# Kernel tuning notes

Hardware: AMD Instinct MI355X
Metric: run time of the kernel (lower is better)

The kernel has to match this reference:

```python
import jax, jax.numpy as jnp
import numpy as np
import math

EMBED = 1024
HEADS = 16
HEAD_DIM = EMBED // HEADS


def setup_inputs() -> dict:
    key = jax.random.key(0)
    ks = jax.random.split(key, 9)
    B, S = 2, 2048
    query = jax.random.normal(ks[0], (B, S, EMBED), dtype=jnp.float32)
    key_t = jax.random.normal(ks[1], (B, S, EMBED), dtype=jnp.float32)
    value = jax.random.normal(ks[2], (B, S, EMBED), dtype=jnp.float32)
    mask = jax.random.randint(ks[3], (B, 1, S, S), 0, 2, dtype=jnp.int32)
    # nn.Linear(head_dim, head_dim, bias=False) weights: [out, in]
    sc = 1.0 / math.sqrt(HEAD_DIM)
    Wq = jax.random.uniform(ks[4], (HEAD_DIM, HEAD_DIM), jnp.float32, -sc, sc)
    Wk = jax.random.uniform(ks[5], (HEAD_DIM, HEAD_DIM), jnp.float32, -sc, sc)
    Wv = jax.random.uniform(ks[6], (HEAD_DIM, HEAD_DIM), jnp.float32, -sc, sc)
    so = 1.0 / math.sqrt(EMBED)
    Wo = jax.random.uniform(ks[7], (EMBED, EMBED), jnp.float32, -so, so)
    bo = jax.random.uniform(ks[8], (EMBED,), jnp.float32, -so, so)
    return {"query": query, "key": key_t, "value": value, "mask": mask,
            "Wq": Wq, "Wk": Wk, "Wv": Wv, "Wo": Wo, "bo": bo}


def reference(query, key, value, mask, Wq, Wk, Wv, Wo, bo):
    B, Sq, E = query.shape
    Sk = key.shape[1]
    H, D = HEADS, HEAD_DIM
    # Faithful raw reshape into heads (as in the torch source, no transpose)
    q = query.reshape(B, H, Sq, D)
    k = key.reshape(B, H, Sk, D)
    v = value.reshape(B, H, Sk, D)
    # per-head_dim Linear (bias-free): x @ W.T
    Q = jnp.einsum('bhsd,ed->bhse', q, Wq)
    K = jnp.einsum('bhsd,ed->bhse', k, Wk)
    V = jnp.einsum('bhsd,ed->bhse', v, Wv)
    scores = jnp.einsum('bhqd,bhkd->bhqk', Q, K)  # [B,H,Sq,Sk]
    scores = jnp.where(mask == 0, jnp.float32(-1e20), scores)
    # NOTE: source divides by sqrt(embed_size), not sqrt(head_dim)
    attn = jax.nn.softmax(scores / jnp.float32(math.sqrt(E)), axis=-1)
    out = jnp.einsum('bhqk,bhkd->bhqd', attn, V).reshape(B, Sq, H * D)
    return out @ Wo.T + bo
```

## Files before the change

kernel.cpp:

```cpp
#include <hip/hip_runtime.h>

typedef __attribute__((ext_vector_type(8))) short short8;
typedef __attribute__((ext_vector_type(4))) float f32x4;
typedef __attribute__((ext_vector_type(2))) int int2v;
typedef __attribute__((ext_vector_type(4))) int int4v;

__device__ __forceinline__ short f2bf(float f) {
  unsigned u = __builtin_bit_cast(unsigned, f);
  u += 0x7fff + ((u >> 16) & 1);
  return (short)(u >> 16);
}

__device__ __forceinline__ int pk2bf(float lo, float hi) {
#if defined(__gfx950__) && __has_builtin(__builtin_amdgcn_cvt_pk_bf16_f32)
  typedef __attribute__((ext_vector_type(2))) __bf16 bf16x2;
  bf16x2 v = __builtin_amdgcn_cvt_pk_bf16_f32(lo, hi);
  return __builtin_bit_cast(int, v);
#else
  return (int)(unsigned short)(short)f2bf(lo) | (((int)f2bf(hi)) << 16);
#endif
}

__device__ __forceinline__ int pktr(float lo, float hi) {
#if __has_builtin(__builtin_amdgcn_perm)
  return (int)__builtin_amdgcn_perm(__builtin_bit_cast(unsigned, hi),
                                    __builtin_bit_cast(unsigned, lo), 0x07060302u);
#else
  return (int)(__builtin_bit_cast(unsigned, lo) >> 16) |
         (int)(__builtin_bit_cast(unsigned, hi) & 0xffff0000u);
#endif
}

__device__ __forceinline__ short8 pack8(f32x4 a, f32x4 b) {
  int4v t;
  t.x = pk2bf(a[0], a[1]);
  t.y = pk2bf(a[2], a[3]);
  t.z = pk2bf(b[0], b[1]);
  t.w = pk2bf(b[2], b[3]);
  return __builtin_bit_cast(short8, t);
}

__device__ __forceinline__ float fand(float p, int m) {
  return __builtin_bit_cast(float, __builtin_bit_cast(int, p) & m);
}

__device__ __forceinline__ int bmask(unsigned w, int bit) {
#if __has_builtin(__builtin_amdgcn_sbfe)
  return __builtin_amdgcn_sbfe((int)w, bit, 1);
#else
  return ((int)(w << (31 - bit))) >> 31;
#endif
}

__device__ __forceinline__ float fexp2(float x) {
#if __has_builtin(__builtin_amdgcn_exp2f)
  return __builtin_amdgcn_exp2f(x);
#else
  return exp2f(x);
#endif
}

__device__ __forceinline__ void glds16(const short* g, short* lbase, int lane) {
#if __has_builtin(__builtin_amdgcn_global_load_lds)
  __builtin_amdgcn_global_load_lds(
      (const __attribute__((address_space(1))) unsigned int*)g,
      (__attribute__((address_space(3))) unsigned int*)lbase, 16, 0, 0);
#else
  *(short8*)(lbase + lane * 8) = *(const short8*)g;
#endif
}

__global__ __launch_bounds__(256) void projqkv(const float* __restrict__ q,
                                               const float* __restrict__ k,
                                               const float* __restrict__ v,
                                               const float* __restrict__ Wq,
                                               const float* __restrict__ Wk,
                                               const float* __restrict__ Wv,
                                               short* __restrict__ Qp,
                                               short* __restrict__ Kp,
                                               short* __restrict__ Vtp) {
  const int bid = blockIdx.x;
  const int tid = threadIdx.x;

  __shared__ short xt[64][72];
  __shared__ short ot[64][72];
  const int mode = bid >> 10;
  const int bt = bid & 1023;
  const float* X;
  const float* W;
  float scale;
  if (mode == 0) { X = q; W = Wq; scale = 0.045084220f; }
  else if (mode == 1) { X = k; W = Wk; scale = 1.0f; }
  else { X = v; W = Wv; scale = 1.0f; }

  const int r0 = bt * 64;
  const int row = tid >> 2, seg = (tid & 3) * 16;
  const f32x4* xs = (const f32x4*)(X + (r0 + row) * 64 + seg);
  const f32x4 x0 = xs[0], x1 = xs[1], x2 = xs[2], x3 = xs[3];
  *(short8*)&xt[row][seg] = pack8(x0, x1);
  *(short8*)&xt[row][seg + 8] = pack8(x2, x3);
  __syncthreads();

  const int lane = tid & 63, wave = tid >> 6;
  const int m16 = lane & 15, quad = lane >> 4;

  const short8 a0 = *(const short8*)&xt[wave * 16 + m16][quad * 8];
  const short8 a1 = *(const short8*)&xt[wave * 16 + m16][32 + quad * 8];

  f32x4 acc[4];
#pragma unroll
  for (int nt = 0; nt < 4; ++nt) {
    const f32x4* wp0 = (const f32x4*)&W[(nt * 16 + m16) * 64 + quad * 8];
    const f32x4* wp1 = (const f32x4*)&W[(nt * 16 + m16) * 64 + 32 + quad * 8];
    const short8 b0 = pack8(wp0[0], wp0[1]);
    const short8 b1 = pack8(wp1[0], wp1[1]);
    f32x4 z = (f32x4){0.f, 0.f, 0.f, 0.f};
    z = __builtin_amdgcn_mfma_f32_16x16x32_bf16(a0, b0, z, 0, 0, 0);
    z = __builtin_amdgcn_mfma_f32_16x16x32_bf16(a1, b1, z, 0, 0, 0);
    acc[nt] = z;
  }

  if (mode != 2) {
#pragma unroll
    for (int nt = 0; nt < 4; ++nt)
#pragma unroll
      for (int r = 0; r < 4; ++r)
        ot[wave * 16 + quad * 4 + r][nt * 16 + m16] = f2bf(acc[nt][r] * scale);
  } else {
#pragma unroll
    for (int nt = 0; nt < 4; ++nt)
#pragma unroll
      for (int r = 0; r < 4; ++r)
        ot[nt * 16 + m16][quad * 8 + (wave & 1) * 4 + r + (wave >> 1) * 32] =
            f2bf(acc[nt][r]);
  }
  __syncthreads();

  const int orow = tid >> 2, opart = tid & 3;
  if (mode != 2) {
    short* dst = (mode == 0 ? Qp : Kp) + (r0 + orow) * 64 + opart * 16;
    *(short8*)&dst[0] = *(const short8*)&ot[orow][opart * 16];
    *(short8*)&dst[8] = *(const short8*)&ot[orow][opart * 16 + 8];
  } else {
    const int bh = r0 >> 11, s0 = r0 & 2047;
    short* dst = Vtp + bh * 131072 + orow * 2048 + s0 + opart * 16;
    *(short8*)&dst[0] = *(const short8*)&ot[orow][opart * 16];
    *(short8*)&dst[8] = *(const short8*)&ot[orow][opart * 16 + 8];
  }
}

__global__ __launch_bounds__(256) void maskwo(const int* __restrict__ mask,
                                              const float* __restrict__ Wo,
                                              short* __restrict__ Wob,
                                              unsigned* __restrict__ mmod) {
  const int bid = blockIdx.x;
  const int tid = threadIdx.x;

  if (bid >= 1024) {
    const int i = ((bid - 1024) * 256 + tid) * 4;
    const f32x4 x = *(const f32x4*)&Wo[i];
    int2v o;
    o.x = pk2bf(x[0], x[1]);
    o.y = pk2bf(x[2], x[3]);
    *(int2v*)&Wob[i] = o;
    return;
  }

  __shared__ __attribute__((aligned(16))) unsigned char mbits[8192];
  const int mb = bid;
  const int kp = mb & 15, bq = mb >> 4;
  const int b_ = bq >> 5, q64 = bq & 31;
  const int* msrc = mask + b_ * 4194304 + q64 * 64 * 2048 + kp * 128;

#pragma unroll
  for (int i = 0; i < 8; ++i) {
    const int idx = tid + i * 256;
    const int row = idx >> 5;
    const int col = (idx * 4) & 127;
    const int4v x = *(const int4v*)(msrc + row * 2048 + col);
    const unsigned w = (unsigned)x.x | ((unsigned)x.y << 8) |
                       ((unsigned)x.z << 16) | ((unsigned)x.w << 24);
    *(unsigned*)(mbits + row * 128 + (col ^ ((row & 7) << 4))) = w;
  }
  __syncthreads();

  const int wv = tid >> 6, qd = (tid >> 4) & 3, m16_ = tid & 15;
  const int row = wv * 16 + m16_;
  const int swz = (row & 7) << 4;
  const unsigned char* rb = mbits + row * 128;
  unsigned d = 0;
#pragma unroll
  for (int hb = 0; hb < 2; ++hb)
#pragma unroll
    for (int grp = 0; grp < 4; ++grp) {
      const unsigned w =
          *(const unsigned*)(rb + ((hb * 64 + grp * 16 + qd * 4) ^ swz));
      const unsigned nib = (((w & 0x01010101u) * 0x01020408u) >> 24) & 0xFu;
      d |= nib << (hb * 16 + grp * 4);
    }
  mmod[mb * 256 + tid] = d;
}

__global__ __launch_bounds__(256) void flash64r(const short* __restrict__ Qp,
                                                const short* __restrict__ Kp,
                                                const short* __restrict__ Vt,
                                                const unsigned* __restrict__ mmod,
                                                short* __restrict__ Ob) {
  __shared__ __attribute__((aligned(16))) short kt0[4096];
  __shared__ __attribute__((aligned(16))) short kt1[4096];
  __shared__ __attribute__((aligned(16))) short vt0[4096];
  __shared__ __attribute__((aligned(16))) short vt1[4096];
  const int tid = threadIdx.x;
  const int bid = blockIdx.x;
  const int local = bid >> 3;
  const int qblk = local & 31;
  const int bh = (bid & 7) * 4 + (local >> 5);
  const int q0 = qblk << 6;
  const int b = bh >> 4;
  const short* Qh = Qp + bh * 131072;
  const short* Kh = Kp + bh * 131072;
  const short* Vh = Vt + bh * 131072;
  const int lane = tid & 63, wave = tid >> 6;
  const int m16 = lane & 15, quad = lane >> 4;
  const int srow = lane >> 3, sj = (lane & 7) ^ srow;
  const int koff = m16 * 128 + ((quad ^ (m16 & 7)) * 16);
  const int koffx = koff ^ 64;
  const unsigned* mq = mmod + ((b * 32 + qblk) * 16) * 256 + wave * 64 + quad * 16 + m16;

  const short onebf = (short)0x3F80;
  const short8 ones = (short8){onebf, onebf, onebf, onebf, onebf, onebf, onebf, onebf};

  short8 aq[2];
#pragma unroll
  for (int h = 0; h < 2; ++h)
    aq[h] = *(const short8*)&Qh[(q0 + wave * 16 + m16) * 64 + h * 32 + quad * 8];

  f32x4 oaccL = (f32x4){0.f, 0.f, 0.f, 0.f};
  f32x4 oacc[4];
#pragma unroll
  for (int dt = 0; dt < 4; ++dt) oacc[dt] = (f32x4){0.f, 0.f, 0.f, 0.f};

  auto stage = [&](short* ktb, short* vtb, int ka) {
#pragma unroll
    for (int t = 0; t < 2; ++t) {
      const int crow = wave * 16 + t * 8;
      glds16(Kh + (ka * 64 + crow + srow) * 64 + sj * 8, ktb + crow * 64, lane);
      glds16(Vh + (crow + srow) * 2048 + ka * 64 + sj * 8, vtb + crow * 64, lane);
    }
  };

  auto compute = [&](const short* ktp, const short* vtp, unsigned mw, int bb) {
    const char* kb_lo = (const char*)ktp + koff;
    const char* kb_hi = (const char*)ktp + koffx;
    const char* vb_lo = (const char*)vtp + koff;
    const char* vb_hi = (const char*)vtp + koffx;
    f32x4 s[4];
    __builtin_amdgcn_s_setprio(1);
#pragma unroll
    for (int grp = 0; grp < 4; ++grp) {
      const short8 kb0 = *(const short8*)(kb_lo + grp * 2048);
      const short8 kb1 = *(const short8*)(kb_hi + grp * 2048);
      f32x4 z = (f32x4){0.f, 0.f, 0.f, 0.f};
      z = __builtin_amdgcn_mfma_f32_16x16x32_bf16(kb0, aq[0], z, 0, 0, 0);
      z = __builtin_amdgcn_mfma_f32_16x16x32_bf16(kb1, aq[1], z, 0, 0, 0);
      s[grp] = z;
    }
    __builtin_amdgcn_s_setprio(0);

    float p[4][4];
#pragma unroll
    for (int grp = 0; grp < 4; ++grp)
#pragma unroll
      for (int r = 0; r < 4; ++r)
        p[grp][r] = fand(fexp2(s[grp][r]), bmask(mw, bb + grp * 4 + r));

    int4v t0, t1;
    t0.x = pktr(p[0][0], p[0][1]);
    t0.y = pktr(p[0][2], p[0][3]);
    t0.z = pktr(p[1][0], p[1][1]);
    t0.w = pktr(p[1][2], p[1][3]);
    t1.x = pktr(p[2][0], p[2][1]);
    t1.y = pktr(p[2][2], p[2][3]);
    t1.z = pktr(p[3][0], p[3][1]);
    t1.w = pktr(p[3][2], p[3][3]);
    const short8 ap0 = __builtin_bit_cast(short8, t0);
    const short8 ap1 = __builtin_bit_cast(short8, t1);

    __builtin_amdgcn_s_setprio(1);
    oaccL = __builtin_amdgcn_mfma_f32_16x16x32_bf16(ap0, ones, oaccL, 0, 0, 0);
    oaccL = __builtin_amdgcn_mfma_f32_16x16x32_bf16(ap1, ones, oaccL, 0, 0, 0);
#pragma unroll
    for (int dt = 0; dt < 4; ++dt) {
      const short8 vb0 = *(const short8*)(vb_lo + dt * 2048);
      const short8 vb1 = *(const short8*)(vb_hi + dt * 2048);
      f32x4 z = oacc[dt];
      z = __builtin_amdgcn_mfma_f32_16x16x32_bf16(ap0, vb0, z, 0, 0, 0);
      z = __builtin_amdgcn_mfma_f32_16x16x32_bf16(ap1, vb1, z, 0, 0, 0);
      oacc[dt] = z;
    }
    __builtin_amdgcn_s_setprio(0);
  };

  unsigned mw = mq[0];
  stage(kt0, vt0, 0);
  stage(kt1, vt1, 1);

  for (int kk = 0; kk < 15; ++kk) {
    const unsigned mwn = mq[(kk + 1) * 256];
    asm volatile("s_waitcnt vmcnt(5)" ::: "memory");
    __builtin_amdgcn_s_barrier();
    compute(kt0, vt0, mw, 0);
    __builtin_amdgcn_s_barrier();
    stage(kt0, vt0, 2 * kk + 2);
    asm volatile("s_waitcnt vmcnt(5)" ::: "memory");
    __builtin_amdgcn_s_barrier();
    compute(kt1, vt1, mw, 16);
    __builtin_amdgcn_s_barrier();
    stage(kt1, vt1, 2 * kk + 3);
    mw = mwn;
  }
  asm volatile("s_waitcnt vmcnt(4)" ::: "memory");
  __builtin_amdgcn_s_barrier();
  compute(kt0, vt0, mw, 0);
  asm volatile("s_waitcnt vmcnt(0)" ::: "memory");
  __builtin_amdgcn_s_barrier();
  compute(kt1, vt1, mw, 16);

  float linv[4];
#pragma unroll
  for (int r = 0; r < 4; ++r) linv[r] = 1.0f / oaccL[r];

  char* const ptB = (char*)kt0;
#pragma unroll
  for (int r = 0; r < 4; ++r) {
    const int row = wave * 16 + quad * 4 + r;
#pragma unroll
    for (int dt = 0; dt < 4; ++dt)
      *(short*)(ptB + row * 128 + ((dt * 32 + m16 * 2) ^ ((row & 7) << 4))) =
          f2bf(oacc[dt][r] * linv[r]);
  }
  asm volatile("s_waitcnt lgkmcnt(0)" ::: "memory");

  const int orow = lane >> 2, opart = lane & 3;
  const int prow = wave * 16 + orow;
  const int oswz = (orow & 7) << 4;
  short* og = Ob + (bh * 2048 + q0 + prow) * 64 + opart * 16;
  *(short8*)&og[0] = *(const short8*)(ptB + prow * 128 + ((opart * 32) ^ oswz));
  *(short8*)&og[8] = *(const short8*)(ptB + prow * 128 + ((opart * 32 + 16) ^ oswz));
}

__global__ __launch_bounds__(256) void outproj(const short* __restrict__ Ob,
                                               const short* __restrict__ Wob,
                                               const float* __restrict__ bo,
                                               float* __restrict__ out) {
  __shared__ __attribute__((aligned(16))) short at0[4096];
  __shared__ __attribute__((aligned(16))) short at1[4096];
  __shared__ __attribute__((aligned(16))) short bt0[8192];
  __shared__ __attribute__((aligned(16))) short bt1[8192];
  const int tid = threadIdx.x;
  const int bid = blockIdx.x;
  const int ct = bid >> 6, rt = bid & 63;
  const int r0 = rt * 64, c0 = ct * 128;
  const int lane = tid & 63, wave = tid >> 6;
  const int mr = (wave >> 1) * 32, nc = (wave & 1) * 64;
  const int m16 = lane & 15, quad = lane >> 4;
  const int srow = lane >> 3, sj = (lane & 7) ^ srow;
  const int mswz = (m16 & 7) << 4;

  f32x4 acc[2][4];
#pragma unroll
  for (int mt = 0; mt < 2; ++mt)
#pragma unroll
    for (int nt = 0; nt < 4; ++nt) acc[mt][nt] = (f32x4){0.f, 0.f, 0.f, 0.f};

  auto stageK = [&](short* atb, short* btb, int kc) {
#pragma unroll
    for (int t = 0; t < 2; ++t) {
      const int crow = wave * 16 + t * 8;
      glds16(Ob + (r0 + crow + srow) * 1024 + kc * 64 + sj * 8, atb + crow * 64, lane);
    }
#pragma unroll
    for (int t = 0; t < 4; ++t) {
      const int crow = wave * 32 + t * 8;
      glds16(Wob + (c0 + crow + srow) * 1024 + kc * 64 + sj * 8, btb + crow * 64, lane);
    }
  };

  auto computeK = [&](const short* atp, const short* btp) {
    const char* atB = (const char*)atp;
    const char* btB = (const char*)btp;
#pragma unroll
    for (int kh = 0; kh < 2; ++kh) {
      short8 af[2], bf[4];
#pragma unroll
      for (int i = 0; i < 2; ++i)
        af[i] = *(const short8*)(atB + (mr + i * 16 + m16) * 128 +
                                 ((kh * 64 + quad * 16) ^ mswz));
#pragma unroll
      for (int j = 0; j < 4; ++j)
        bf[j] = *(const short8*)(btB + (nc + j * 16 + m16) * 128 +
                                 ((kh * 64 + quad * 16) ^ mswz));
      __builtin_amdgcn_s_setprio(1);
#pragma unroll
      for (int mt = 0; mt < 2; ++mt)
#pragma unroll
        for (int nt = 0; nt < 4; ++nt)
          acc[mt][nt] = __builtin_amdgcn_mfma_f32_16x16x32_bf16(af[mt], bf[nt],
                                                                acc[mt][nt], 0, 0, 0);
      __builtin_amdgcn_s_setprio(0);
    }
  };

  stageK(at0, bt0, 0);
  stageK(at1, bt1, 1);
  for (int kc = 0; kc < 14; ++kc) {
    short* atb = (kc & 1) ? at1 : at0;
    short* btb = (kc & 1) ? bt1 : bt0;
    asm volatile("s_waitcnt vmcnt(6)" ::: "memory");
    __builtin_amdgcn_s_barrier();
    computeK(atb, btb);
    __builtin_amdgcn_s_barrier();
    stageK(atb, btb, kc + 2);
  }
  asm volatile("s_waitcnt vmcnt(6)" ::: "memory");
  __builtin_amdgcn_s_barrier();
  computeK(at0, bt0);
  asm volatile("s_waitcnt vmcnt(0)" ::: "memory");
  __builtin_amdgcn_s_barrier();
  computeK(at1, bt1);

#pragma unroll
  for (int nt = 0; nt < 4; ++nt) {
    const int col = c0 + nc + nt * 16 + m16;
    const float bias = bo[col];
#pragma unroll
    for (int mt = 0; mt < 2; ++mt)
#pragma unroll
      for (int rr2 = 0; rr2 < 4; ++rr2)
        out[(r0 + mr + mt * 16 + quad * 4 + rr2) * 1024 + col] = acc[mt][nt][rr2] + bias;
  }
}

extern "C" void kernel_launch(void* const* d_in, const int* in_sizes, int n_in,
                              void* d_out, int out_size, void* d_ws, size_t ws_size,
                              hipStream_t stream) {
  const float* query = (const float*)d_in[0];
  const float* key = (const float*)d_in[1];
  const float* value = (const float*)d_in[2];
  const int* mask = (const int*)d_in[3];
  const float* Wq = (const float*)d_in[4];
  const float* Wk = (const float*)d_in[5];
  const float* Wv = (const float*)d_in[6];
  const float* Wo = (const float*)d_in[7];
  const float* bo = (const float*)d_in[8];
  float* out = (float*)d_out;

  char* ws = (char*)d_ws;
  short* Qp = (short*)(ws);
  short* Kp = (short*)(ws + 8388608);
  short* Vt = (short*)(ws + 16777216);
  short* Ob = (short*)(ws + 25165824);
  short* Wob = (short*)(ws + 41943040);
  unsigned* mmod = (unsigned*)(ws + 44564480);

  projqkv<<<3072, 256, 0, stream>>>(query, key, value, Wq, Wk, Wv, Qp, Kp, Vt);
  maskwo<<<2048, 256, 0, stream>>>(mask, Wo, Wob, mmod);
  flash64r<<<1024, 256, 0, stream>>>(Qp, Kp, Vt, mmod, Ob);
  outproj<<<512, 256, 0, stream>>>(Ob, Wob, bo, out);
}
```

Baseline: 219.5 us.

## Split flash waves 2x2 over query and key halves; merge prep kernels

Restructures the attention kernel so each wave handles 32 query rows against half of each 64-key tile instead of 16 rows against the full tile. Each K/V fragment read from shared memory then feeds two query groups, cutting LDS reads per MFMA. Partial outputs and row sums from the two key-half waves are combined through shared memory at the end, which adds extra barriers. The mask-packing layout is changed to match, and the projection and mask/Wo-conversion kernels are merged into one launch to save a kernel boundary.

```diff
diff --git a/kernel.cpp b/kernel.cpp
--- a/kernel.cpp
+++ b/kernel.cpp
@@ -70,17 +70,71 @@
 #endif
 }
 
-__global__ __launch_bounds__(256) void projqkv(const float* __restrict__ q,
-                                               const float* __restrict__ k,
-                                               const float* __restrict__ v,
-                                               const float* __restrict__ Wq,
-                                               const float* __restrict__ Wk,
-                                               const float* __restrict__ Wv,
-                                               short* __restrict__ Qp,
-                                               short* __restrict__ Kp,
-                                               short* __restrict__ Vtp) {
+__global__ __launch_bounds__(256) void prep(const float* __restrict__ q,
+                                            const float* __restrict__ k,
+                                            const float* __restrict__ v,
+                                            const float* __restrict__ Wq,
+                                            const float* __restrict__ Wk,
+                                            const float* __restrict__ Wv,
+                                            const float* __restrict__ Wo,
+                                            const int* __restrict__ mask,
+                                            short* __restrict__ Qp,
+                                            short* __restrict__ Kp,
+                                            short* __restrict__ Vtp,
+                                            short* __restrict__ Wob,
+                                            unsigned* __restrict__ mmod) {
   const int bid = blockIdx.x;
   const int tid = threadIdx.x;
+
+  if (bid >= 4096) {
+    const int i = ((bid - 4096) * 256 + tid) * 4;
+    const f32x4 x = *(const f32x4*)&Wo[i];
+    int2v o;
+    o.x = pk2bf(x[0], x[1]);
+    o.y = pk2bf(x[2], x[3]);
+    *(int2v*)&Wob[i] = o;
+    return;
+  }
+  if (bid >= 3072) {
+    __shared__ __attribute__((aligned(16))) unsigned char mbits[8192];
+    const int mb = bid - 3072;
+    const int kp = mb & 15, bq = mb >> 4;
+    const int b_ = bq >> 5, q64 = bq & 31;
+    const int* msrc = mask + b_ * 4194304 + q64 * 64 * 2048 + kp * 128;
+
+#pragma unroll
+    for (int i = 0; i < 8; ++i) {
+      const int idx = tid + i * 256;
+      const int row = idx >> 5;
+      const int col = (idx * 4) & 127;
+      const int4v x = *(const int4v*)(msrc + row * 2048 + col);
+      const unsigned w = (unsigned)x.x | ((unsigned)x.y << 8) |
+                         ((unsigned)x.z << 16) | ((unsigned)x.w << 24);
+      *(unsigned*)(mbits + row * 128 + (col ^ ((row & 7) << 4))) = w;
+    }
+    __syncthreads();
+
+    const int qh_ = tid >> 7, kh_ = (tid >> 6) & 1;
+    const int qd = (tid >> 4) & 3, m16_ = tid & 15;
+    unsigned d = 0;
+#pragma unroll
+    for (int hb = 0; hb < 2; ++hb)
+#pragma unroll
+      for (int qg = 0; qg < 2; ++qg) {
+        const int row = qh_ * 32 + qg * 16 + m16_;
+        const unsigned char* rb = mbits + row * 128;
+        const int swz = (row & 7) << 4;
+#pragma unroll
+        for (int kg = 0; kg < 2; ++kg) {
+          const unsigned w = *(const unsigned*)(
+              rb + ((hb * 64 + kh_ * 32 + kg * 16 + qd * 4) ^ swz));
+          const unsigned nib = (((w & 0x01010101u) * 0x01020408u) >> 24) & 0xFu;
+          d |= nib << (hb * 16 + qg * 8 + kg * 4);
+        }
+      }
+    mmod[mb * 256 + tid] = d;
+    return;
+  }
 
   __shared__ short xt[64][72];
   __shared__ short ot[64][72];
@@ -149,59 +203,7 @@
   }
 }
 
-__global__ __launch_bounds__(256) void maskwo(const int* __restrict__ mask,
-                                              const float* __restrict__ Wo,
-                                              short* __restrict__ Wob,
-                                              unsigned* __restrict__ mmod) {
-  const int bid = blockIdx.x;
-  const int tid = threadIdx.x;
-
-  if (bid >= 1024) {
-    const int i = ((bid - 1024) * 256 + tid) * 4;
-    const f32x4 x = *(const f32x4*)&Wo[i];
-    int2v o;
-    o.x = pk2bf(x[0], x[1]);
-    o.y = pk2bf(x[2], x[3]);
-    *(int2v*)&Wob[i] = o;
-    return;
-  }
-
-  __shared__ __attribute__((aligned(16))) unsigned char mbits[8192];
-  const int mb = bid;
-  const int kp = mb & 15, bq = mb >> 4;
-  const int b_ = bq >> 5, q64 = bq & 31;
-  const int* msrc = mask + b_ * 4194304 + q64 * 64 * 2048 + kp * 128;
-
-#pragma unroll
-  for (int i = 0; i < 8; ++i) {
-    const int idx = tid + i * 256;
-    const int row = idx >> 5;
-    const int col = (idx * 4) & 127;
-    const int4v x = *(const int4v*)(msrc + row * 2048 + col);
-    const unsigned w = (unsigned)x.x | ((unsigned)x.y << 8) |
-                       ((unsigned)x.z << 16) | ((unsigned)x.w << 24);
-    *(unsigned*)(mbits + row * 128 + (col ^ ((row & 7) << 4))) = w;
-  }
-  __syncthreads();
-
-  const int wv = tid >> 6, qd = (tid >> 4) & 3, m16_ = tid & 15;
-  const int row = wv * 16 + m16_;
-  const int swz = (row & 7) << 4;
-  const unsigned char* rb = mbits + row * 128;
-  unsigned d = 0;
-#pragma unroll
-  for (int hb = 0; hb < 2; ++hb)
-#pragma unroll
-    for (int grp = 0; grp < 4; ++grp) {
-      const unsigned w =
-          *(const unsigned*)(rb + ((hb * 64 + grp * 16 + qd * 4) ^ swz));
-      const unsigned nib = (((w & 0x01010101u) * 0x01020408u) >> 24) & 0xFu;
-      d |= nib << (hb * 16 + grp * 4);
-    }
-  mmod[mb * 256 + tid] = d;
-}
-
-__global__ __launch_bounds__(256) void flash64r(const short* __restrict__ Qp,
+__global__ __launch_bounds__(256) void flash64q(const short* __restrict__ Qp,
                                                 const short* __restrict__ Kp,
                                                 const short* __restrict__ Vt,
                                                 const unsigned* __restrict__ mmod,
@@ -221,24 +223,33 @@
   const short* Kh = Kp + bh * 131072;
   const short* Vh = Vt + bh * 131072;
   const int lane = tid & 63, wave = tid >> 6;
+  const int qh = wave >> 1, kh = wave & 1;
   const int m16 = lane & 15, quad = lane >> 4;
   const int srow = lane >> 3, sj = (lane & 7) ^ srow;
-  const int koff = m16 * 128 + ((quad ^ (m16 & 7)) * 16);
-  const int koffx = koff ^ 64;
-  const unsigned* mq = mmod + ((b * 32 + qblk) * 16) * 256 + wave * 64 + quad * 16 + m16;
+  const int mlow = m16 & 7;
+  const int kqoff = kh * 4096 + m16 * 128 + ((quad ^ mlow) * 16);
+  const int pvoff = m16 * 128 + ((((kh << 2) | quad) ^ mlow) * 16);
+  const unsigned* mq = mmod + ((b * 32 + qblk) * 16) * 256 + tid;
 
   const short onebf = (short)0x3F80;
   const short8 ones = (short8){onebf, onebf, onebf, onebf, onebf, onebf, onebf, onebf};
 
-  short8 aq[2];
-#pragma unroll
-  for (int h = 0; h < 2; ++h)
-    aq[h] = *(const short8*)&Qh[(q0 + wave * 16 + m16) * 64 + h * 32 + quad * 8];
-
-  f32x4 oaccL = (f32x4){0.f, 0.f, 0.f, 0.f};
-  f32x4 oacc[4];
-#pragma unroll
-  for (int dt = 0; dt < 4; ++dt) oacc[dt] = (f32x4){0.f, 0.f, 0.f, 0.f};
+  short8 aq[2][2];
+#pragma unroll
+  for (int qg = 0; qg < 2; ++qg)
+#pragma unroll
+    for (int h = 0; h < 2; ++h)
+      aq[qg][h] = *(const short8*)&Qh[(q0 + qh * 32 + qg * 16 + m16) * 64 +
+                                      h * 32 + quad * 8];
+
+  f32x4 oaccL[2];
+  oaccL[0] = (f32x4){0.f, 0.f, 0.f, 0.f};
+  oaccL[1] = (f32x4){0.f, 0.f, 0.f, 0.f};
+  f32x4 oacc[2][4];
+#pragma unroll
+  for (int qg = 0; qg < 2; ++qg)
+#pragma unroll
+    for (int dt = 0; dt < 4; ++dt) oacc[qg][dt] = (f32x4){0.f, 0.f, 0.f, 0.f};
 
   auto stage = [&](short* ktb, short* vtb, int ka) {
 #pragma unroll
@@ -250,53 +261,55 @@
   };
 
   auto compute = [&](const short* ktp, const short* vtp, unsigned mw, int bb) {
-    const char* kb_lo = (const char*)ktp + koff;
-    const char* kb_hi = (const char*)ktp + koffx;
-    const char* vb_lo = (const char*)vtp + koff;
-    const char* vb_hi = (const char*)vtp + koffx;
-    f32x4 s[4];
+    const char* ktB = (const char*)ktp;
+    const char* vtB = (const char*)vtp;
+    f32x4 s[2][2];
     __builtin_amdgcn_s_setprio(1);
 #pragma unroll
-    for (int grp = 0; grp < 4; ++grp) {
-      const short8 kb0 = *(const short8*)(kb_lo + grp * 2048);
-      const short8 kb1 = *(const short8*)(kb_hi + grp * 2048);
-      f32x4 z = (f32x4){0.f, 0.f, 0.f, 0.f};
-      z = __builtin_amdgcn_mfma_f32_16x16x32_bf16(kb0, aq[0], z, 0, 0, 0);
-      z = __builtin_amdgcn_mfma_f32_16x16x32_bf16(kb1, aq[1], z, 0, 0, 0);
-      s[grp] = z;
+    for (int kg = 0; kg < 2; ++kg) {
+      const short8 kb0 = *(const short8*)(ktB + kqoff + kg * 2048);
+      const short8 kb1 = *(const short8*)(ktB + (kqoff ^ 64) + kg * 2048);
+#pragma unroll
+      for (int qg = 0; qg < 2; ++qg) {
+        f32x4 z = (f32x4){0.f, 0.f, 0.f, 0.f};
+        z = __builtin_amdgcn_mfma_f32_16x16x32_bf16(kb0, aq[qg][0], z, 0, 0, 0);
+        z = __builtin_amdgcn_mfma_f32_16x16x32_bf16(kb1, aq[qg][1], z, 0, 0, 0);
+        s[qg][kg] = z;
+      }
     }
     __builtin_amdgcn_s_setprio(0);
 
-    float p[4][4];
-#pragma unroll
-    for (int grp = 0; grp < 4; ++grp)
-#pragma unroll
-      for (int r = 0; r < 4; ++r)
-        p[grp][r] = fand(fexp2(s[grp][r]), bmask(mw, bb + grp * 4 + r));
-
-    int4v t0, t1;
-    t0.x = pktr(p[0][0], p[0][1]);
-    t0.y = pktr(p[0][2], p[0][3]);
-    t0.z = pktr(p[1][0], p[1][1]);
-    t0.w = pktr(p[1][2], p[1][3]);
-    t1.x = pktr(p[2][0], p[2][1]);
-    t1.y = pktr(p[2][2], p[2][3]);
-    t1.z = pktr(p[3][0], p[3][1]);
-    t1.w = pktr(p[3][2], p[3][3]);
-    const short8 ap0 = __builtin_bit_cast(short8, t0);
-    const short8 ap1 = __builtin_bit_cast(short8, t1);
+    float p[2][2][4];
+#pragma unroll
+    for (int qg = 0; qg < 2; ++qg)
+#pragma unroll
+      for (int kg = 0; kg < 2; ++kg)
+#pragma unroll
+        for (int r = 0; r < 4; ++r)
+          p[qg][kg][r] =
+              fand(fexp2(s[qg][kg][r]), bmask(mw, bb + qg * 8 + kg * 4 + r));
+
+    short8 ap[2];
+#pragma unroll
+    for (int qg = 0; qg < 2; ++qg) {
+      int4v t;
+      t.x = pktr(p[qg][0][0], p[qg][0][1]);
+      t.y = pktr(p[qg][0][2], p[qg][0][3]);
+      t.z = pktr(p[qg][1][0], p[qg][1][1]);
+      t.w = pktr(p[qg][1][2], p[qg][1][3]);
+      ap[qg] = __builtin_bit_cast(short8, t);
+    }
 
     __builtin_amdgcn_s_setprio(1);
-    oaccL = __builtin_amdgcn_mfma_f32_16x16x32_bf16(ap0, ones, oaccL, 0, 0, 0);
-    oaccL = __builtin_amdgcn_mfma_f32_16x16x32_bf16(ap1, ones, oaccL, 0, 0, 0);
+    oaccL[0] = __builtin_amdgcn_mfma_f32_16x16x32_bf16(ap[0], ones, oaccL[0], 0, 0, 0);
+    oaccL[1] = __builtin_amdgcn_mfma_f32_16x16x32_bf16(ap[1], ones, oaccL[1], 0, 0, 0);
 #pragma unroll
     for (int dt = 0; dt < 4; ++dt) {
-      const short8 vb0 = *(const short8*)(vb_lo + dt * 2048);
-      const short8 vb1 = *(const short8*)(vb_hi + dt * 2048);
-      f32x4 z = oacc[dt];
-      z = __builtin_amdgcn_mfma_f32_16x16x32_bf16(ap0, vb0, z, 0, 0, 0);
-      z = __builtin_amdgcn_mfma_f32_16x16x32_bf16(ap1, vb1, z, 0, 0, 0);
-      oacc[dt] = z;
+      const short8 vb = *(const short8*)(vtB + pvoff + dt * 2048);
+#pragma unroll
+      for (int qg = 0; qg < 2; ++qg)
+        oacc[qg][dt] =
+            __builtin_amdgcn_mfma_f32_16x16x32_bf16(ap[qg], vb, oacc[qg][dt], 0, 0, 0);
     }
     __builtin_amdgcn_s_setprio(0);
   };
@@ -325,28 +338,57 @@
   asm volatile("s_waitcnt vmcnt(0)" ::: "memory");
   __builtin_amdgcn_s_barrier();
   compute(kt1, vt1, mw, 16);
-
-  float linv[4];
-#pragma unroll
-  for (int r = 0; r < 4; ++r) linv[r] = 1.0f / oaccL[r];
-
-  char* const ptB = (char*)kt0;
-#pragma unroll
-  for (int r = 0; r < 4; ++r) {
-    const int row = wave * 16 + quad * 4 + r;
-#pragma unroll
-    for (int dt = 0; dt < 4; ++dt)
-      *(short*)(ptB + row * 128 + ((dt * 32 + m16 * 2) ^ ((row & 7) << 4))) =
-          f2bf(oacc[dt][r] * linv[r]);
+  __builtin_amdgcn_s_barrier();
+
+  char* const P0 = (char*)kt0;
+  char* const P1 = (char*)kt1;
+  float* const lx = (float*)vt0;
+  char* const pC = qh ? P1 : P0;
+
+  if (kh == 1) {
+#pragma unroll
+    for (int qg = 0; qg < 2; ++qg)
+#pragma unroll
+      for (int r = 0; r < 4; ++r) {
+        const int ql = qg * 16 + quad * 4 + r;
+#pragma unroll
+        for (int dt = 0; dt < 4; ++dt)
+          *(float*)(pC + ql * 256 + (((dt * 16 + m16) * 4) ^ ((ql & 7) << 4))) =
+              oacc[qg][dt][r];
+        if (m16 == 0) lx[qh * 32 + ql] = oaccL[qg][r];
+      }
   }
   asm volatile("s_waitcnt lgkmcnt(0)" ::: "memory");
+  __builtin_amdgcn_s_barrier();
+
+  char* const ob = (char*)vt1;
+  if (kh == 0) {
+#pragma unroll
+    for (int qg = 0; qg < 2; ++qg)
+#pragma unroll
+      for (int r = 0; r < 4; ++r) {
+        const int ql = qg * 16 + quad * 4 + r;
+        const float lt = oaccL[qg][r] + lx[qh * 32 + ql];
+        const float inv = 1.0f / lt;
+        const int qrow = qh * 32 + ql;
+#pragma unroll
+        for (int dt = 0; dt < 4; ++dt) {
+          const float part =
+              *(const float*)(pC + ql * 256 + (((dt * 16 + m16) * 4) ^ ((ql & 7) << 4)));
+          *(short*)(ob + qrow * 128 + ((dt * 32 + m16 * 2) ^ ((qrow & 7) << 4))) =
+              f2bf((oacc[qg][dt][r] + part) * inv);
+        }
+      }
+  }
+  asm volatile("s_waitcnt lgkmcnt(0)" ::: "memory");
+  __builtin_amdgcn_s_barrier();
 
   const int orow = lane >> 2, opart = lane & 3;
   const int prow = wave * 16 + orow;
   const int oswz = (orow & 7) << 4;
   short* og = Ob + (bh * 2048 + q0 + prow) * 64 + opart * 16;
-  *(short8*)&og[0] = *(const short8*)(ptB + prow * 128 + ((opart * 32) ^ oswz));
-  *(short8*)&og[8] = *(const short8*)(ptB + prow * 128 + ((opart * 32 + 16) ^ oswz));
+  *(short8*)&og[0] = *(const short8*)(ob + prow * 128 + ((opart * 32) ^ oswz));
+  *(short8*)&og[8] = *(const short8*)(ob + prow * 128 + ((opart * 32 + 16) ^ oswz));
 }
 
 __global__ __launch_bounds__(256) void outproj(const short* __restrict__ Ob,
@@ -463,8 +505,8 @@
   short* Wob = (short*)(ws + 41943040);
   unsigned* mmod = (unsigned*)(ws + 44564480);
 
-  projqkv<<<3072, 256, 0, stream>>>(query, key, value, Wq, Wk, Wv, Qp, Kp, Vt);
-  maskwo<<<2048, 256, 0, stream>>>(mask, Wo, Wob, mmod);
-  flash64r<<<1024, 256, 0, stream>>>(Qp, Kp, Vt, mmod, Ob);
+  prep<<<5120, 256, 0, stream>>>(query, key, value, Wq, Wk, Wv, Wo, mask,
+                                 Qp, Kp, Vt, Wob, mmod);
+  flash64q<<<1024, 256, 0, stream>>>(Qp, Kp, Vt, mmod, Ob);
   outproj<<<512, 256, 0, stream>>>(Ob, Wob, bo, out);
 }
```

After: 213.1 us. -2.9%, faster.
